# Performance work log

Measured on AMD Instinct MI355X. Metric: run time of the kernel, lower is better.

Reference implementation:

```python
import jax, jax.numpy as jnp
import numpy as np

EMBED = 768
HEADS = 12
HEAD_DIM = EMBED // HEADS
STREAMS = 4
SK_ITERS = 20
MLP_HIDDEN = 3072
EPS_SK = 1e-8
EPS_LN = 1e-5


def setup_inputs() -> dict:
    key = jax.random.key(0)
    ks = jax.random.split(key, 16)
    w = lambda k, shape: (jax.random.normal(k, shape, dtype=jnp.float32) * 0.02)
    return {
        "x": jax.random.normal(ks[0], (8, 1024, EMBED), dtype=jnp.float32),
        "ln1_g": jnp.ones((EMBED,), jnp.float32),
        "ln1_b": jnp.zeros((EMBED,), jnp.float32),
        "ln2_g": jnp.ones((EMBED,), jnp.float32),
        "ln2_b": jnp.zeros((EMBED,), jnp.float32),
        "qkv_w": w(ks[1], (3 * EMBED, EMBED)),
        "qkv_b": jnp.zeros((3 * EMBED,), jnp.float32),
        "proj_w": w(ks[2], (EMBED, EMBED)),
        "proj_b": jnp.zeros((EMBED,), jnp.float32),
        "fc1_w": w(ks[3], (MLP_HIDDEN, EMBED)),
        "fc1_b": jnp.zeros((MLP_HIDDEN,), jnp.float32),
        "fc2_w": w(ks[4], (EMBED, MLP_HIDDEN)),
        "fc2_b": jnp.zeros((EMBED,), jnp.float32),
        "a_hres": w(ks[5], (STREAMS, STREAMS)),
        "a_hpre": w(ks[6], (STREAMS,)),
        "a_hpost": w(ks[7], (STREAMS,)),
        "m_hres": w(ks[8], (STREAMS, STREAMS)),
        "m_hpre": w(ks[9], (STREAMS,)),
        "m_hpost": w(ks[10], (STREAMS,)),
    }


def layernorm(x, g, b):
    mu = x.mean(-1, keepdims=True)
    var = ((x - mu) ** 2).mean(-1, keepdims=True)
    return (x - mu) * jax.lax.rsqrt(var + EPS_LN) * g + b


def sinkhorn_knopp(logits):
    # logits: (n, n) -> doubly-stochastic (n, n); batch expansion in torch is redundant
    A = jnp.exp(logits)
    for _ in range(SK_ITERS):
        A = A / (A.sum(-1, keepdims=True) + EPS_SK)
        A = A / (A.sum(-2, keepdims=True) + EPS_SK)
    return A


def attention(x, qkv_w, qkv_b, proj_w, proj_b):
    B, N, D = x.shape
    qkv = x @ qkv_w.T + qkv_b                      # (B, N, 3D)
    qkv = qkv.reshape(B, N, 3, HEADS, HEAD_DIM)
    q, k, v = jnp.moveaxis(qkv, 2, 0)              # each (B, N, H, hd)
    scale = HEAD_DIM ** -0.5
    scores = jnp.einsum('bqhd,bkhd->bhqk', q, k) * scale
    attn = jax.nn.softmax(scores, axis=-1)
    out = jnp.einsum('bhqk,bkhd->bqhd', attn, v).reshape(B, N, D)
    return out @ proj_w.T + proj_b


def mlp(x, fc1_w, fc1_b, fc2_w, fc2_b):
    h = jax.nn.gelu(x @ fc1_w.T + fc1_b, approximate=False)
    return h @ fc2_w.T + fc2_b


def mhc(x, hres_logits, hpre_logits, hpost_logits, transform_fn):
    B, L, D = x.shape
    n, c = STREAMS, D // STREAMS
    xs = x.reshape(B, L, n, c)
    H_res = sinkhorn_knopp(hres_logits)            # (n, n)
    H_pre = jax.nn.softmax(hpre_logits)            # (n,)
    H_post = jax.nn.softmax(hpost_logits)          # (n,)
    x_pre = jnp.einsum('n,blnc->blc', H_pre, xs)   # weighted sum over streams
    x_pre_full = jnp.tile(x_pre, (1, 1, n))        # (B, L, D)
    t = transform_fn(x_pre_full)
    t_mean = t.reshape(B, L, n, c).mean(axis=2)    # (B, L, c)
    out = (jnp.einsum('nm,blmc->blnc', H_res, xs)
           + H_post[None, None, :, None] * t_mean[:, :, None, :])
    return out.reshape(B, L, D)


def reference(x, ln1_g, ln1_b, ln2_g, ln2_b, qkv_w, qkv_b, proj_w, proj_b,
              fc1_w, fc1_b, fc2_w, fc2_b,
              a_hres, a_hpre, a_hpost, m_hres, m_hpre, m_hpost):
    x = mhc(x, a_hres, a_hpre, a_hpost,
            lambda h: attention(layernorm(h, ln1_g, ln1_b), qkv_w, qkv_b, proj_w, proj_b))
    x = mhc(x, m_hres, m_hpre, m_hpost,
            lambda h: mlp(layernorm(h, ln2_g, ln2_b), fc1_w, fc1_b, fc2_w, fc2_b))
    return x
```

## Files before the change

kernel.cpp:

```cpp
#include <hip/hip_runtime.h>
#include <hip/hip_bf16.h>
#include <cstdint>
#include <cstddef>

#define EMBED 768
#define STREAMS 4
#define CHUNK 192
#define HEADS 12
#define HD 64
#define SEQ 1024
#define BATCH 8
#define TOKENS (BATCH * SEQ)
#define MLPH 3072

typedef __bf16 bf16;
typedef __bf16 bf16x4 __attribute__((ext_vector_type(4)));
typedef __bf16 bf16x8 __attribute__((ext_vector_type(8)));
typedef float f32x4 __attribute__((ext_vector_type(4)));
typedef float f32x16 __attribute__((ext_vector_type(16)));

#define GLDS16(gp, lp)                                                        \
  __builtin_amdgcn_global_load_lds(                                           \
      (const __attribute__((address_space(1))) void*)(gp),                    \
      (__attribute__((address_space(3))) void*)(lp), 16, 0, 0)

#define BARRIER() do { asm volatile("" ::: "memory");                         \
  __builtin_amdgcn_s_barrier(); asm volatile("" ::: "memory"); } while (0)

#define CVT_NQ 442368
#define CVT_NP 147456
#define CVT_N1 589824
#define CVT_TOT (CVT_NQ + CVT_NP + 2 * CVT_N1)
__global__ __launch_bounds__(256) void cvt_hprep_kernel(
    const float* __restrict__ qw, const float* __restrict__ pw,
    const float* __restrict__ f1w, const float* __restrict__ f2w,
    bf16* __restrict__ Wq, bf16* __restrict__ Wp,
    bf16* __restrict__ W1, bf16* __restrict__ W2,
    const float* ar, const float* ap, const float* ao,
    const float* mr, const float* mp, const float* mo, float* HS) {
  if (blockIdx.x == 2048) {
    if (threadIdx.x != 0) return;
    const float* L[2] = {ar, mr};
    const float* P[2] = {ap, mp};
    const float* O[2] = {ao, mo};
    for (int s = 0; s < 2; ++s) {
      float A[16];
      for (int i = 0; i < 16; ++i) A[i] = expf(L[s][i]);
      for (int it = 0; it < 20; ++it) {
        for (int r = 0; r < 4; ++r) {
          float rs = A[4*r] + A[4*r+1] + A[4*r+2] + A[4*r+3] + 1e-8f;
          for (int c = 0; c < 4; ++c) A[4*r+c] /= rs;
        }
        for (int c = 0; c < 4; ++c) {
          float cs = A[c] + A[4+c] + A[8+c] + A[12+c] + 1e-8f;
          for (int r = 0; r < 4; ++r) A[4*r+c] /= cs;
        }
      }
      float* dst = HS + s * 24;
      for (int i = 0; i < 16; ++i) dst[i] = A[i];
      {
        float m = fmaxf(fmaxf(P[s][0], P[s][1]), fmaxf(P[s][2], P[s][3]));
        float e[4], t = 0.f;
        for (int i = 0; i < 4; ++i) { e[i] = expf(P[s][i] - m); t += e[i]; }
        for (int i = 0; i < 4; ++i) dst[16 + i] = e[i] / t;
      }
      {
        float m = fmaxf(fmaxf(O[s][0], O[s][1]), fmaxf(O[s][2], O[s][3]));
        float e[4], t = 0.f;
        for (int i = 0; i < 4; ++i) { e[i] = expf(O[s][i] - m); t += e[i]; }
        for (int i = 0; i < 4; ++i) dst[20 + i] = e[i] / t;
      }
    }
    return;
  }
  int i = blockIdx.x * 256 + threadIdx.x;
  const int st = 2048 * 256;
  for (; i < CVT_TOT; i += st) {
    const float* src; bf16* dst; int off;
    if (i < CVT_NQ)                      { src = qw;  dst = Wq; off = i; }
    else if (i < CVT_NQ + CVT_NP)        { src = pw;  dst = Wp; off = i - CVT_NQ; }
    else if (i < CVT_NQ + CVT_NP + CVT_N1){ src = f1w; dst = W1; off = i - CVT_NQ - CVT_NP; }
    else                                 { src = f2w; dst = W2; off = i - CVT_NQ - CVT_NP - CVT_N1; }
    const float4 v = ((const float4*)src)[off];
    bf16x4 o = {(bf16)v.x, (bf16)v.y, (bf16)v.z, (bf16)v.w};
    *(bf16x4*)(dst + (size_t)off * 4) = o;
  }
}

__global__ __launch_bounds__(256) void preln_kernel(
    const float* __restrict__ x, const float* __restrict__ H,
    const float* __restrict__ g, const float* __restrict__ b,
    bf16* __restrict__ out) {
  const int t = blockIdx.x;
  const float* xr = x + (size_t)t * EMBED;
  __shared__ float s[CHUNK];
  __shared__ float part[8];
  __shared__ float red[2];
  const int tid = threadIdx.x;
  float sv = 0.f;
  if (tid < CHUNK) {
    sv = H[0]*xr[tid] + H[1]*xr[CHUNK+tid] + H[2]*xr[2*CHUNK+tid] + H[3]*xr[3*CHUNK+tid];
    s[tid] = sv;
  }
  float sum = sv, sq = sv * sv;
  #pragma unroll
  for (int m = 32; m > 0; m >>= 1) {
    sum += __shfl_down(sum, m);
    sq  += __shfl_down(sq, m);
  }
  if ((tid & 63) == 0) { part[tid >> 6] = sum; part[4 + (tid >> 6)] = sq; }
  __syncthreads();
  if (tid == 0) {
    float S = part[0] + part[1] + part[2] + part[3];
    float Q = part[4] + part[5] + part[6] + part[7];
    float mu = S * (1.f / CHUNK);
    float var = Q * (1.f / CHUNK) - mu * mu;
    red[0] = mu;
    red[1] = rsqrtf(var + 1e-5f);
  }
  __syncthreads();
  const float mu = red[0], rs = red[1];
  bf16* orow = out + (size_t)t * EMBED;
  #pragma unroll
  for (int r = 0; r < 3; ++r) {
    const int d = tid + r * 256;
    const float v = (s[d % CHUNK] - mu) * rs * g[d] + b[d];
    orow[d] = (bf16)v;
  }
}

template <int GELU, int KSPLIT>
__global__ __launch_bounds__(256, 2) void gemm_bt(
    const bf16* __restrict__ A, const bf16* __restrict__ B,
    const float* __restrict__ bias, bf16* __restrict__ C0,
    bf16* __restrict__ C1, int M, int N, int K) {
  constexpr int BM = 128, BN = 128, BK = 32;
  __shared__ bf16 sA[3][BM * BK];
  __shared__ bf16 sB[3][BN * BK];
  const int tid  = threadIdx.x;
  const int lane = tid & 63;
  const int nwg = gridDim.x * gridDim.y;
  int Lw = blockIdx.y * gridDim.x + blockIdx.x;
  Lw = (Lw & 7) * (nwg >> 3) + (Lw >> 3);
  const int bm = (Lw / gridDim.x) * BM;
  const int bn = (Lw % gridDim.x) * BN;
  const int wave = tid >> 6;
  const int wr = (wave >> 1) * 64;
  const int wc = (wave & 1) * 64;
  f32x16 acc[2][2] = {};
  const int tr = tid >> 2;
  const int gt = tid & 3;
  const int gsw = (gt ^ ((tr >> 1) & 3)) * 8;
  const int kbeg = (KSPLIT > 1) ? blockIdx.z * (K / KSPLIT) : 0;
  const bf16* Ag = A + (size_t)(bm + tr) * K + kbeg + gsw;
  const bf16* Bg = B + (size_t)(bn + tr) * K + kbeg + gsw;
  const int lofs = tr * BK + gt * 8;
  const int r31 = lane & 31, rh = lane >> 5;
  const int asw = (r31 >> 1) & 3;
  const int nst = K / KSPLIT / BK;
#define STAGE(buf, t)                                                         \
  do { const int bk_ = (t) * BK;                                              \
    GLDS16(Ag + bk_, sA[buf] + lofs);                                         \
    GLDS16(Ag + (size_t)64 * K + bk_, sA[buf] + lofs + 64 * BK);              \
    GLDS16(Bg + bk_, sB[buf] + lofs);                                         \
    GLDS16(Bg + (size_t)64 * K + bk_, sB[buf] + lofs + 64 * BK);              \
  } while (0)
  STAGE(0, 0);
  STAGE(1, 1);
  int cur = 0;
  for (int t = 0; t < nst; ++t) {
    if (t + 2 < nst) {
      const int nb = cur + 2 >= 3 ? cur - 1 : cur + 2;
      STAGE(nb, t + 2);
      asm volatile("s_waitcnt vmcnt(8)" ::: "memory");
    } else if (t + 1 < nst) {
      asm volatile("s_waitcnt vmcnt(4)" ::: "memory");
    } else {
      asm volatile("s_waitcnt vmcnt(0)" ::: "memory");
    }
    BARRIER();
    bf16x8 af[2][2], bfr[2][2];
    #pragma unroll
    for (int ks = 0; ks < 2; ++ks) {
      const int pos = ((ks * 2 + rh) ^ asw) * 8;
      #pragma unroll
      for (int i = 0; i < 2; ++i) {
        af[i][ks]  = *(const bf16x8*)(sA[cur] + (wr + i * 32 + r31) * BK + pos);
        bfr[i][ks] = *(const bf16x8*)(sB[cur] + (wc + i * 32 + r31) * BK + pos);
      }
    }
    #pragma unroll
    for (int ks = 0; ks < 2; ++ks)
      #pragma unroll
      for (int i = 0; i < 2; ++i)
        #pragma unroll
        for (int j = 0; j < 2; ++j)
          acc[i][j] = __builtin_amdgcn_mfma_f32_32x32x16_bf16(af[i][ks], bfr[j][ks], acc[i][j], 0, 0, 0);
    BARRIER();
    cur = cur == 2 ? 0 : cur + 1;
  }
#undef STAGE
  const bool second = (KSPLIT > 1) && (blockIdx.z != 0);
  bf16* Co = second ? C1 : C0;
  #pragma unroll
  for (int j = 0; j < 2; ++j) {
    const int col = bn + wc + j * 32 + r31;
    const float bv = second ? 0.f : bias[col];
    #pragma unroll
    for (int i = 0; i < 2; ++i) {
      const int row0 = bm + wr + i * 32 + 4 * rh;
      #pragma unroll
      for (int reg = 0; reg < 16; ++reg) {
        const int row = row0 + (reg & 3) + 8 * (reg >> 2);
        float v = acc[i][j][reg] + bv;
        if (GELU) {
          float u = 0.7978845608f * (v + 0.044715f * v * v * v);
          u = fmaxf(fminf(u, 15.f), -15.f);
          const float e = __expf(-2.f * u);
          v = v / (1.f + e);
        }
        Co[(size_t)row * N + col] = (bf16)v;
      }
    }
  }
}

__global__ __launch_bounds__(256) void vt_kernel(const bf16* __restrict__ qkv,
                                                 bf16* __restrict__ VT) {
  const int tt = blockIdx.x;
  const int bh = blockIdx.y;
  const int bb = bh / HEADS;
  const int h = bh - bb * HEADS;
  __shared__ bf16 sT[64 * 64];
  const int t = threadIdx.x;
  const int srow = t >> 3;
  const int g = t & 7;
  const int gs = ((g ^ (srow & 7)) * 8);
  const bf16* Vg = qkv + ((size_t)(bb * SEQ + tt * 64 + srow)) * 2304 + 1536 + h * 64;
  GLDS16(Vg + gs, sT + srow * 64 + g * 8);
  GLDS16(Vg + (size_t)32 * 2304 + gs, sT + (32 + srow) * 64 + g * 8);
  __syncthreads();
  const int hd = t >> 2;
  const int tg = (t & 3) * 16;
  bf16 tmp[16];
  #pragma unroll
  for (int j = 0; j < 16; ++j) {
    const int tok = tg + j;
    tmp[j] = sT[tok * 64 + (hd ^ ((tok & 7) << 3))];
  }
  bf16* op = VT + (size_t)bh * (HD * SEQ) + (size_t)hd * SEQ + tt * 64 + tg;
  *(bf16x8*)(op) = *(const bf16x8*)(tmp);
  *(bf16x8*)(op + 8) = *(const bf16x8*)(tmp + 8);
}

__global__ __launch_bounds__(512) void attn_kernel(
    const bf16* __restrict__ qkv, const bf16* __restrict__ VT,
    bf16* __restrict__ out) {
  const int lin = blockIdx.x;
  const int qt = (lin >> 3) & 7;
  const int bh = (lin & 7) + 8 * (lin >> 6);
  const int bb = bh / HEADS;
  const int h = bh - bb * HEADS;
  const int tid = threadIdx.x;
  const int lane = tid & 63;
  const int wave = tid >> 6;
  const size_t tokBase = (size_t)bb * SEQ;
  const int q0 = qt * 128;

  __shared__ bf16 sQ[128 * 64];
  __shared__ bf16 sK[2][64 * 64];
  __shared__ bf16 sV[2][80 * 64];
  __shared__ bf16 sP[8][16 * 64];

  for (int idx = tid; idx < 16 * 64; idx += 512) {
    const bf16 v = (idx < 64) ? (bf16)1.f : (bf16)0.f;
    sV[0][64 * 64 + idx] = v;
    sV[1][64 * 64 + idx] = v;
  }

  {
    #pragma unroll
    for (int kq = 0; kq < 2; ++kq) {
      const int slot = tid + kq * 512;
      const int qr = slot >> 3;
      const int qg = slot & 7;
      const bf16* Qg = qkv + (tokBase + q0 + qr) * 2304 + h * 64;
      GLDS16(Qg + ((qg ^ (qr & 7)) * 8), sQ + qr * 64 + qg * 8);
    }
  }
  const int srow = tid >> 3;
  const int g = tid & 7;
  const int gs = ((g ^ (srow & 7)) * 8);
  const bf16* Kbase = qkv + tokBase * 2304 + 768 + h * 64;
  const bf16* Vbase = VT + (size_t)bh * (HD * SEQ);
  GLDS16(Kbase + (size_t)srow * 2304 + gs, sK[0] + srow * 64 + g * 8);
  GLDS16(Vbase + (size_t)srow * SEQ + gs, sV[0] + srow * 64 + g * 8);
  __syncthreads();

  const int l15 = lane & 15, hi = lane >> 4;
  const int ksw = (l15 & 7) << 3;
  bf16x8 qf[2];
  {
    const int qrow = wave * 16 + l15;
    const int qsw = (qrow & 7) << 3;
    #pragma unroll
    for (int ks = 0; ks < 2; ++ks)
      qf[ks] = *(const bf16x8*)(sQ + qrow * 64 + ((hi * 8 + ks * 32) ^ qsw));
  }

  f32x4 o[5] = {};

  for (int it = 0; it < SEQ / 64; ++it) {
    const int cur = it & 1;
    if (it + 1 < SEQ / 64) {
      const int kb = (it + 1) * 64;
      GLDS16(Kbase + (size_t)(kb + srow) * 2304 + gs, sK[cur ^ 1] + srow * 64 + g * 8);
      GLDS16(Vbase + (size_t)srow * SEQ + kb + gs, sV[cur ^ 1] + srow * 64 + g * 8);
      asm volatile("s_waitcnt vmcnt(2)" ::: "memory");
    } else {
      asm volatile("s_waitcnt vmcnt(0)" ::: "memory");
    }
    BARRIER();
    f32x4 s[4];
    __builtin_amdgcn_s_setprio(1);
    #pragma unroll
    for (int nj = 0; nj < 4; ++nj) {
      s[nj] = (f32x4){0.f, 0.f, 0.f, 0.f};
      #pragma unroll
      for (int ks = 0; ks < 2; ++ks) {
        bf16x8 kf = *(const bf16x8*)(sK[cur] + (nj * 16 + l15) * 64 + ((hi * 8 + ks * 32) ^ ksw));
        s[nj] = __builtin_amdgcn_mfma_f32_16x16x32_bf16(qf[ks], kf, s[nj], 0, 0, 0);
      }
    }
    __builtin_amdgcn_s_setprio(0);
    bf16* Pw = sP[wave];
    #pragma unroll
    for (int r = 0; r < 4; ++r) {
      const int prow = hi * 4 + r;
      const int psw = (prow & 7) << 3;
      #pragma unroll
      for (int nj = 0; nj < 4; ++nj)
        Pw[prow * 64 + ((nj * 16 + l15) ^ psw)] = (bf16)__expf(s[nj][r] * 0.125f);
    }
    __builtin_amdgcn_s_setprio(1);
    #pragma unroll
    for (int ks = 0; ks < 2; ++ks) {
      bf16x8 pa = *(const bf16x8*)(Pw + l15 * 64 + ((hi * 8 + ks * 32) ^ ksw));
      #pragma unroll
      for (int nj = 0; nj < 5; ++nj) {
        bf16x8 vb = *(const bf16x8*)(sV[cur] + (nj * 16 + l15) * 64 + ((hi * 8 + ks * 32) ^ ksw));
        o[nj] = __builtin_amdgcn_mfma_f32_16x16x32_bf16(pa, vb, o[nj], 0, 0, 0);
      }
    }
    __builtin_amdgcn_s_setprio(0);
    BARRIER();
  }
  #pragma unroll
  for (int r = 0; r < 4; ++r) {
    const float lsum = __shfl(o[4][r], hi << 4, 64);
    const float inv = 1.f / lsum;
    const size_t row = tokBase + q0 + wave * 16 + hi * 4 + r;
    bf16* orow = out + row * EMBED + h * 64;
    #pragma unroll
    for (int nj = 0; nj < 4; ++nj)
      orow[nj * 16 + l15] = (bf16)(o[nj][r] * inv);
  }
}

template <int TWO>
__global__ __launch_bounds__(256) void combine_preln_kernel(
    const float* __restrict__ x, const bf16* __restrict__ t,
    const bf16* __restrict__ t2,
    const float* __restrict__ Hres, const float* __restrict__ Hpost,
    const float* __restrict__ Hpre2,
    const float* __restrict__ g2, const float* __restrict__ b2,
    float* __restrict__ X2, bf16* __restrict__ LN) {
  const int tok = blockIdx.x;
  const int tid = threadIdx.x;
  __shared__ float s[CHUNK];
  __shared__ float part[8];
  __shared__ float red[2];
  float sv = 0.f;
  if (tid < CHUNK) {
    const float* xr = x + (size_t)tok * EMBED + tid;
    const bf16* tr = t + (size_t)tok * EMBED + tid;
    const float x0 = xr[0], x1 = xr[CHUNK], x2v = xr[2 * CHUNK], x3 = xr[3 * CHUNK];
    float tm = (float)tr[0] + (float)tr[CHUNK] + (float)tr[2 * CHUNK] + (float)tr[3 * CHUNK];
    if (TWO) {
      const bf16* t2r = t2 + (size_t)tok * EMBED + tid;
      tm += (float)t2r[0] + (float)t2r[CHUNK] + (float)t2r[2 * CHUNK] + (float)t2r[3 * CHUNK];
    }
    tm *= 0.25f;
    float* orow = X2 + (size_t)tok * EMBED + tid;
    #pragma unroll
    for (int n = 0; n < 4; ++n) {
      const float v = Hres[4*n+0]*x0 + Hres[4*n+1]*x1 + Hres[4*n+2]*x2v + Hres[4*n+3]*x3
                    + Hpost[n] * tm;
      orow[n * CHUNK] = v;
      sv += Hpre2[n] * v;
    }
    s[tid] = sv;
  }
  float sum = sv, sq = sv * sv;
  #pragma unroll
  for (int m = 32; m > 0; m >>= 1) {
    sum += __shfl_down(sum, m);
    sq  += __shfl_down(sq, m);
  }
  if ((tid & 63) == 0) { part[tid >> 6] = sum; part[4 + (tid >> 6)] = sq; }
  __syncthreads();
  if (tid == 0) {
    float S = part[0] + part[1] + part[2] + part[3];
    float Q = part[4] + part[5] + part[6] + part[7];
    float mu = S * (1.f / CHUNK);
    float var = Q * (1.f / CHUNK) - mu * mu;
    red[0] = mu;
    red[1] = rsqrtf(var + 1e-5f);
  }
  __syncthreads();
  const float mu = red[0], rs = red[1];
  bf16* lrow = LN + (size_t)tok * EMBED;
  #pragma unroll
  for (int r = 0; r < 3; ++r) {
    const int d = tid + r * 256;
    lrow[d] = (bf16)((s[d % CHUNK] - mu) * rs * g2[d] + b2[d]);
  }
}

template <int TWO>
__global__ void combine_kernel(const float* __restrict__ xs, const bf16* __restrict__ t,
                               const bf16* __restrict__ t2,
                               const float* __restrict__ Hres, const float* __restrict__ Hpost,
                               float* __restrict__ outp) {
  const int idx = blockIdx.x * 256 + threadIdx.x;
  if (idx >= TOKENS * CHUNK) return;
  const int tok = idx / CHUNK;
  const int c = idx - tok * CHUNK;
  const float* xr = xs + (size_t)tok * EMBED + c;
  const bf16* tr = t + (size_t)tok * EMBED + c;
  const float x0 = xr[0], x1 = xr[CHUNK], x2 = xr[2 * CHUNK], x3 = xr[3 * CHUNK];
  float tm = (float)tr[0] + (float)tr[CHUNK] + (float)tr[2 * CHUNK] + (float)tr[3 * CHUNK];
  if (TWO) {
    const bf16* t2r = t2 + (size_t)tok * EMBED + c;
    tm += (float)t2r[0] + (float)t2r[CHUNK] + (float)t2r[2 * CHUNK] + (float)t2r[3 * CHUNK];
  }
  tm *= 0.25f;
  #pragma unroll
  for (int n = 0; n < 4; ++n) {
    const float v = Hres[4*n+0]*x0 + Hres[4*n+1]*x1 + Hres[4*n+2]*x2 + Hres[4*n+3]*x3
                  + Hpost[n] * tm;
    outp[(size_t)tok * EMBED + n * CHUNK + c] = v;
  }
}

extern "C" void kernel_launch(void* const* d_in, const int* in_sizes, int n_in,
                              void* d_out, int out_size, void* d_ws, size_t ws_size,
                              hipStream_t stream) {
  const float* x       = (const float*)d_in[0];
  const float* ln1_g   = (const float*)d_in[1];
  const float* ln1_b   = (const float*)d_in[2];
  const float* ln2_g   = (const float*)d_in[3];
  const float* ln2_b   = (const float*)d_in[4];
  const float* qkv_w   = (const float*)d_in[5];
  const float* qkv_b   = (const float*)d_in[6];
  const float* proj_w  = (const float*)d_in[7];
  const float* proj_b  = (const float*)d_in[8];
  const float* fc1_w   = (const float*)d_in[9];
  const float* fc1_b   = (const float*)d_in[10];
  const float* fc2_w   = (const float*)d_in[11];
  const float* fc2_b   = (const float*)d_in[12];
  const float* a_hres  = (const float*)d_in[13];
  const float* a_hpre  = (const float*)d_in[14];
  const float* a_hpost = (const float*)d_in[15];
  const float* m_hres  = (const float*)d_in[16];
  const float* m_hpre  = (const float*)d_in[17];
  const float* m_hpost = (const float*)d_in[18];

  char* ws = (char*)d_ws;
  float* HS = (float*)(ws);
  bf16* Wq  = (bf16*)(ws + 1024);
  bf16* Wp  = (bf16*)(ws + 1024 + 3538944);
  bf16* W1  = (bf16*)(ws + 1024 + 3538944 + 1179648);
  bf16* W2  = (bf16*)(ws + 1024 + 3538944 + 1179648 + 4718592);
  bf16* LN  = (bf16*)(ws + 14156800);
  bf16* T   = (bf16*)(ws + 26739712);
  bf16* PT  = (bf16*)(ws + 39322624);
  float* X2 = (float*)(ws + 51905536);
  bf16* QKV = (bf16*)(ws + 77071360);
  bf16* AO  = (bf16*)(ws + 114820096);
  bf16* Hm  = (bf16*)(ws + 77071360);
  bf16* VT  = LN;

  cvt_hprep_kernel<<<2049, 256, 0, stream>>>(
      qkv_w, proj_w, fc1_w, fc2_w, Wq, Wp, W1, W2,
      a_hres, a_hpre, a_hpost, m_hres, m_hpre, m_hpost, HS);

  preln_kernel<<<TOKENS, 256, 0, stream>>>(x, HS + 16, ln1_g, ln1_b, LN);
  gemm_bt<0, 1><<<dim3(2304 / 128, TOKENS / 128), 256, 0, stream>>>(
      LN, Wq, qkv_b, QKV, nullptr, TOKENS, 2304, 768);
  vt_kernel<<<dim3(16, 96), 256, 0, stream>>>(QKV, VT);
  attn_kernel<<<768, 512, 0, stream>>>(QKV, VT, AO);
  gemm_bt<0, 2><<<dim3(768 / 128, TOKENS / 128, 2), 256, 0, stream>>>(
      AO, Wp, proj_b, T, PT, TOKENS, 768, 768);
  combine_preln_kernel<1><<<TOKENS, 256, 0, stream>>>(
      x, T, PT, HS + 0, HS + 20, HS + 24 + 16, ln2_g, ln2_b, X2, LN);

  gemm_bt<1, 1><<<dim3(3072 / 128, TOKENS / 128), 256, 0, stream>>>(
      LN, W1, fc1_b, Hm, nullptr, TOKENS, 3072, 768);
  gemm_bt<0, 2><<<dim3(768 / 128, TOKENS / 128, 2), 256, 0, stream>>>(
      Hm, W2, fc2_b, T, PT, TOKENS, 768, 3072);
  combine_kernel<1><<<(TOKENS * CHUNK + 255) / 256, 256, 0, stream>>>(
      X2, T, PT, HS + 24, HS + 24 + 20, (float*)d_out);
}
```

Before: 312.9 us.

## Fuse first pre-LN into weight-convert kernel and remap GEMM tile schedule

Merges the first stream-mix plus LayerNorm kernel into the weight-conversion/H-prep kernel. Each LN block recomputes the H_pre softmax locally so it no longer depends on the H-prep block, which removes one launch and lets LN blocks run alongside the weight conversion. Separately, the GEMM workgroup-to-tile mapping now assigns each XCD-strided group a contiguous band of rows and walks the columns within it. This is meant to improve L2 reuse of the A operand. The new tile mapping assumes gridDim.y is divisible by 8.

```diff
diff --git a/kernel.cpp b/kernel.cpp
--- a/kernel.cpp
+++ b/kernel.cpp
@@ -31,15 +31,64 @@
 #define CVT_NP 147456
 #define CVT_N1 589824
 #define CVT_TOT (CVT_NQ + CVT_NP + 2 * CVT_N1)
-__global__ __launch_bounds__(256) void cvt_hprep_kernel(
+__global__ __launch_bounds__(256) void head_kernel(
+    const float* __restrict__ x, const float* __restrict__ ln1_g,
+    const float* __restrict__ ln1_b, bf16* __restrict__ LN,
     const float* __restrict__ qw, const float* __restrict__ pw,
     const float* __restrict__ f1w, const float* __restrict__ f2w,
     bf16* __restrict__ Wq, bf16* __restrict__ Wp,
     bf16* __restrict__ W1, bf16* __restrict__ W2,
     const float* ar, const float* ap, const float* ao,
     const float* mr, const float* mp, const float* mo, float* HS) {
-  if (blockIdx.x == 2048) {
-    if (threadIdx.x != 0) return;
+  const int tid = threadIdx.x;
+  if (blockIdx.x < TOKENS) {
+    const int t = blockIdx.x;
+    const float* xr = x + (size_t)t * EMBED;
+    __shared__ float s[CHUNK];
+    __shared__ float part[8];
+    __shared__ float red[2];
+    float H0, H1, H2, H3;
+    {
+      const float p0 = ap[0], p1 = ap[1], p2 = ap[2], p3 = ap[3];
+      const float m = fmaxf(fmaxf(p0, p1), fmaxf(p2, p3));
+      const float e0 = __expf(p0 - m), e1 = __expf(p1 - m),
+                  e2 = __expf(p2 - m), e3 = __expf(p3 - m);
+      const float inv = 1.f / (e0 + e1 + e2 + e3);
+      H0 = e0 * inv; H1 = e1 * inv; H2 = e2 * inv; H3 = e3 * inv;
+    }
+    float sv = 0.f;
+    if (tid < CHUNK) {
+      sv = H0*xr[tid] + H1*xr[CHUNK+tid] + H2*xr[2*CHUNK+tid] + H3*xr[3*CHUNK+tid];
+      s[tid] = sv;
+    }
+    float sum = sv, sq = sv * sv;
+    #pragma unroll
+    for (int m = 32; m > 0; m >>= 1) {
+      sum += __shfl_down(sum, m);
+      sq  += __shfl_down(sq, m);
+    }
+    if ((tid & 63) == 0) { part[tid >> 6] = sum; part[4 + (tid >> 6)] = sq; }
+    __syncthreads();
+    if (tid == 0) {
+      float S = part[0] + part[1] + part[2] + part[3];
+      float Q = part[4] + part[5] + part[6] + part[7];
+      float mu = S * (1.f / CHUNK);
+      float var = Q * (1.f / CHUNK) - mu * mu;
+      red[0] = mu;
+      red[1] = rsqrtf(var + 1e-5f);
+    }
+    __syncthreads();
+    const float mu = red[0], rs = red[1];
+    bf16* orow = LN + (size_t)t * EMBED;
+    #pragma unroll
+    for (int r = 0; r < 3; ++r) {
+      const int d = tid + r * 256;
+      orow[d] = (bf16)((s[d % CHUNK] - mu) * rs * ln1_g[d] + ln1_b[d]);
+    }
+    return;
+  }
+  if (blockIdx.x == TOKENS + 2048) {
+    if (tid != 0) return;
     const float* L[2] = {ar, mr};
     const float* P[2] = {ap, mp};
     const float* O[2] = {ao, mo};
@@ -73,7 +122,7 @@
     }
     return;
   }
-  int i = blockIdx.x * 256 + threadIdx.x;
+  int i = (blockIdx.x - TOKENS) * 256 + tid;
   const int st = 2048 * 256;
   for (; i < CVT_TOT; i += st) {
     const float* src; bf16* dst; int off;
@@ -87,48 +136,6 @@
   }
 }
 
-__global__ __launch_bounds__(256) void preln_kernel(
-    const float* __restrict__ x, const float* __restrict__ H,
-    const float* __restrict__ g, const float* __restrict__ b,
-    bf16* __restrict__ out) {
-  const int t = blockIdx.x;
-  const float* xr = x + (size_t)t * EMBED;
-  __shared__ float s[CHUNK];
-  __shared__ float part[8];
-  __shared__ float red[2];
-  const int tid = threadIdx.x;
-  float sv = 0.f;
-  if (tid < CHUNK) {
-    sv = H[0]*xr[tid] + H[1]*xr[CHUNK+tid] + H[2]*xr[2*CHUNK+tid] + H[3]*xr[3*CHUNK+tid];
-    s[tid] = sv;
-  }
-  float sum = sv, sq = sv * sv;
-  #pragma unroll
-  for (int m = 32; m > 0; m >>= 1) {
-    sum += __shfl_down(sum, m);
-    sq  += __shfl_down(sq, m);
-  }
-  if ((tid & 63) == 0) { part[tid >> 6] = sum; part[4 + (tid >> 6)] = sq; }
-  __syncthreads();
-  if (tid == 0) {
-    float S = part[0] + part[1] + part[2] + part[3];
-    float Q = part[4] + part[5] + part[6] + part[7];
-    float mu = S * (1.f / CHUNK);
-    float var = Q * (1.f / CHUNK) - mu * mu;
-    red[0] = mu;
-    red[1] = rsqrtf(var + 1e-5f);
-  }
-  __syncthreads();
-  const float mu = red[0], rs = red[1];
-  bf16* orow = out + (size_t)t * EMBED;
-  #pragma unroll
-  for (int r = 0; r < 3; ++r) {
-    const int d = tid + r * 256;
-    const float v = (s[d % CHUNK] - mu) * rs * g[d] + b[d];
-    orow[d] = (bf16)v;
-  }
-}
-
 template <int GELU, int KSPLIT>
 __global__ __launch_bounds__(256, 2) void gemm_bt(
     const bf16* __restrict__ A, const bf16* __restrict__ B,
@@ -139,11 +146,13 @@
   __shared__ bf16 sB[3][BN * BK];
   const int tid  = threadIdx.x;
   const int lane = tid & 63;
-  const int nwg = gridDim.x * gridDim.y;
-  int Lw = blockIdx.y * gridDim.x + blockIdx.x;
-  Lw = (Lw & 7) * (nwg >> 3) + (Lw >> 3);
-  const int bm = (Lw / gridDim.x) * BM;
-  const int bn = (Lw % gridDim.x) * BN;
+  const int Lw = blockIdx.y * gridDim.x + blockIdx.x;
+  const int bandRows = gridDim.y >> 3;
+  const int j = Lw >> 3;
+  const int colIdx = j / bandRows;
+  const int rowLoc = j - colIdx * bandRows;
+  const int bm = ((Lw & 7) * bandRows + rowLoc) * BM;
+  const int bn = colIdx * BN;
   const int wave = tid >> 6;
   const int wr = (wave >> 1) * 64;
   const int wc = (wave & 1) * 64;
@@ -194,8 +203,8 @@
       #pragma unroll
       for (int i = 0; i < 2; ++i)
         #pragma unroll
-        for (int j = 0; j < 2; ++j)
-          acc[i][j] = __builtin_amdgcn_mfma_f32_32x32x16_bf16(af[i][ks], bfr[j][ks], acc[i][j], 0, 0, 0);
+        for (int j2 = 0; j2 < 2; ++j2)
+          acc[i][j2] = __builtin_amdgcn_mfma_f32_32x32x16_bf16(af[i][ks], bfr[j2][ks], acc[i][j2], 0, 0, 0);
     BARRIER();
     cur = cur == 2 ? 0 : cur + 1;
   }
@@ -203,8 +212,8 @@
   const bool second = (KSPLIT > 1) && (blockIdx.z != 0);
   bf16* Co = second ? C1 : C0;
   #pragma unroll
-  for (int j = 0; j < 2; ++j) {
-    const int col = bn + wc + j * 32 + r31;
+  for (int j2 = 0; j2 < 2; ++j2) {
+    const int col = bn + wc + j2 * 32 + r31;
     const float bv = second ? 0.f : bias[col];
     #pragma unroll
     for (int i = 0; i < 2; ++i) {
@@ -212,7 +221,7 @@
       #pragma unroll
       for (int reg = 0; reg < 16; ++reg) {
         const int row = row0 + (reg & 3) + 8 * (reg >> 2);
-        float v = acc[i][j][reg] + bv;
+        float v = acc[i][j2][reg] + bv;
         if (GELU) {
           float u = 0.7978845608f * (v + 0.044715f * v * v * v);
           u = fmaxf(fminf(u, 15.f), -15.f);
@@ -491,11 +500,11 @@
   bf16* Hm  = (bf16*)(ws + 77071360);
   bf16* VT  = LN;
 
-  cvt_hprep_kernel<<<2049, 256, 0, stream>>>(
+  head_kernel<<<TOKENS + 2049, 256, 0, stream>>>(
+      x, ln1_g, ln1_b, LN,
       qkv_w, proj_w, fc1_w, fc2_w, Wq, Wp, W1, W2,
       a_hres, a_hpre, a_hpost, m_hres, m_hpre, m_hpost, HS);
 
-  preln_kernel<<<TOKENS, 256, 0, stream>>>(x, HS + 16, ln1_g, ln1_b, LN);
   gemm_bt<0, 1><<<dim3(2304 / 128, TOKENS / 128), 256, 0, stream>>>(
       LN, Wq, qkv_b, QKV, nullptr, TOKENS, 2304, 768);
   vt_kernel<<<dim3(16, 96), 256, 0, stream>>>(QKV, VT);
```

Measured after the change: 312.2 us. About the same (-0.2%).
